# Kernel optimization log

Measured on AMD Instinct MI355X. Metric: run time of the kernel, lower is better.

Reference implementation:

```python
import jax, jax.numpy as jnp
import numpy as np
from jax import lax

DEPTH_MAX = 6.0
NBINS = 100


def _minpool2d(x):
    # torch: -max_pool2d(-x, 5, 1, 2)  (max_pool pads with -inf => minpool pads with +inf)
    return lax.reduce_window(x, jnp.inf, lax.min, (1, 5, 5), (1, 1, 1),
                             [(0, 0), (2, 2), (2, 2)])


def _maxpool3d(x):
    return lax.reduce_window(x, -jnp.inf, lax.max, (1, 5, 5, 5), (1, 1, 1, 1),
                             [(0, 0), (2, 2), (2, 2), (2, 2)])


def _stuff_padding(row, maxvec):
    # fill zeros of `row` with the first nonzero element of `maxvec`
    v = maxvec[jnp.argmax(maxvec != 0)]  # if all-zero, argmax->0, v=0 (no-op fill)
    return jnp.where(row == 0, v, row)


def _find_none(a):
    # Sequential nearest-nonzero fill: for each zero (left->right), set it to
    # max(min nonzero on the left incl. previous fills, min nonzero on the right
    # of the ORIGINAL array). Expressed as a parallel suffix-min + lax.scan.
    aval = jnp.where(a != 0, a, jnp.inf)
    rev = lax.cummin(aval[::-1])[::-1]
    suf = jnp.concatenate([rev[1:], jnp.full((1,), jnp.inf, a.dtype)])  # min of a[i+1:]

    def step(m, xs):
        ai, si = xs
        l = jnp.where(jnp.isinf(m), 0.0, m)
        r = jnp.where(jnp.isinf(si), 0.0, si)
        val = jnp.where(ai == 0, jnp.maximum(l, r), ai)
        m = jnp.where(val != 0, jnp.minimum(m, val), m)
        return m, val

    _, out = lax.scan(step, jnp.array(jnp.inf, a.dtype), (a, suf))
    return out


def _forward(semantic2d, depth, occupancy2d, kept, mapping):
    B, K, H, W = semantic2d.shape
    D = kept.shape[1]
    sem = jnp.argmax(semantic2d, axis=1)               # [B,H,W]
    feats_sm = jax.nn.softmax(semantic2d, axis=1)      # [B,K,H,W]

    depth = lax.stop_gradient(depth)                   # pred['depth'].detach()
    depth = jnp.minimum(depth, DEPTH_MAX)              # clamp to depth_max
    depth_index = (depth / DEPTH_MAX * 100.0).astype(jnp.int32)  # [B,1,H,W]
    bins = jnp.arange(NBINS, dtype=jnp.int32)[None, :, None, None]

    # stuff mask: erosion (min-pool 5x5) of (semantic >= 10)
    stuff = _minpool2d((sem >= 10).astype(depth.dtype)) > 0.5    # [B,H,W] bool
    stuff_depth = depth[:, 0] * stuff                            # [B,H,W]
    stuff_x_max = stuff_depth.max(axis=1)                        # [B,W]
    stuff_y_max = stuff_depth.max(axis=2)                        # [B,H]

    pad_v = jax.vmap(_stuff_padding)
    sd = stuff_depth
    sd = sd.at[:, 0].set(pad_v(stuff_depth[:, 0], stuff_y_max))
    sd = sd.at[:, -1].set(pad_v(stuff_depth[:, -1], stuff_y_max[:, ::-1]))
    sd = sd.at[:, :, 0].set(pad_v(stuff_depth[:, :, 0], stuff_x_max))
    sd = sd.at[:, :, -1].set(pad_v(stuff_depth[:, :, -1], stuff_x_max[:, ::-1]))

    stuff_x = jax.vmap(_find_none)(sd.max(axis=1))   # [B,W]
    stuff_y = jax.vmap(_find_none)(sd.max(axis=2))   # [B,H]

    # per-pixel max depth: min(stuff_x[b, x], stuff_y[b, y])
    depth_max = jnp.minimum(stuff_x[:, None, None, :], stuff_y[:, None, :, None])  # [B,1,H,W]
    depth_max_bins = (depth_max / DEPTH_MAX * 100.0).astype(jnp.int32)

    depth_feat = (bins - depth_index).astype(depth.dtype) / 100.0 * DEPTH_MAX  # [B,100,H,W]
    depth_feat = jnp.stack([jnp.sign(depth_feat), jnp.abs(depth_feat)], axis=1)  # [B,2,100,H,W]

    depth_weight_kept = (bins > depth_index - 3) & (bins < depth_max_bins + 5)  # [B,100,H,W]
    depth_weight = jax.nn.sigmoid(occupancy2d) * depth_weight_kept

    # voxel -> pixel/bin gather: mapping columns are (batch, x, y, depth_m)
    b_idx = mapping[..., 0].astype(jnp.int32)
    x_idx = mapping[..., 1].astype(jnp.int32)
    y_idx = mapping[..., 2].astype(jnp.int32)
    d_idx = (mapping[..., 3] * 100.0 / DEPTH_MAX).astype(jnp.int32)
    feat_kept = kept & depth_weight_kept[b_idx, d_idx, y_idx, x_idx]  # [B,D,D,D]

    features = jnp.concatenate([
        jnp.broadcast_to(feats_sm[:, :, None], (B, K, NBINS, H, W)),
        depth_weight[:, None],
        depth_feat,
    ], axis=1)  # [B, K+3, 100, H, W]

    # padding voxels: dilation of feat_kept within kept, coords snapped to even
    padding_kept = (_maxpool3d(feat_kept.astype(jnp.float32)) > 0.5) & kept
    batch_point = padding_kept.reshape(B, -1).sum(-1)
    padding_kept = padding_kept.at[:, 127, 127, 127].set(
        jnp.where(batch_point == 0, True, padding_kept[:, 127, 127, 127]))
    padding_kept = padding_kept & ~feat_kept
    blocks = padding_kept.reshape(B, D // 2, 2, D // 2, 2, D // 2, 2).any(axis=(2, 4, 6))
    padding_even = jnp.zeros_like(padding_kept).at[:, ::2, ::2, ::2].set(blocks)

    union = feat_kept | padding_even          # occupied sparse coords (dense form)
    mask = _maxpool3d(union.astype(jnp.float32)) > 0.5
    return features, feat_kept, mask


def setup_inputs() -> dict:
    key = jax.random.key(0)
    ks = jax.random.split(key, 7)
    B, K, H, W, D = 2, 12, 120, 160, 128
    semantic2d = jax.random.normal(ks[0], (B, K, H, W), jnp.float32)
    depth = jax.random.uniform(ks[1], (B, 1, H, W), jnp.float32) * 8.0  # some > depth_max
    occupancy2d = jax.random.normal(ks[2], (B, 100, H, W), jnp.float32)
    kept = jax.random.uniform(ks[3], (B, D, D, D)) < 0.05
    b_col = jnp.broadcast_to(jnp.arange(B, dtype=jnp.float32)[:, None, None, None], (B, D, D, D))
    x_col = jax.random.randint(ks[4], (B, D, D, D), 0, W).astype(jnp.float32)
    y_col = jax.random.randint(ks[5], (B, D, D, D), 0, H).astype(jnp.float32)
    d_col = jax.random.uniform(ks[6], (B, D, D, D)) * (DEPTH_MAX - 1e-3)
    mapping = jnp.stack([b_col, x_col, y_col, d_col], axis=-1)  # [B,D,D,D,4]
    return {"semantic2d": semantic2d, "depth": depth, "occupancy2d": occupancy2d,
            "kept": kept, "mapping": mapping}


def reference(semantic2d, depth, occupancy2d, kept, mapping):
    return _forward(semantic2d, depth, occupancy2d, kept, mapping)
```

## Files before the change

### kernel.cpp

```cpp
#include <hip/hip_runtime.h>
#include <cmath>

#define BB 2
#define KK 12
#define HH 120
#define WW 160
#define HW (HH*WW)
#define DD 128
#define NB 100
#define DMAXF 6.0f
#define NLINES (BB*DD*DD)
#define NVOX (BB*DD*DD*DD)

__global__ void k1_pixel(const float* __restrict__ sem2d, const float* __restrict__ depth,
                         float* __restrict__ feats_sm, float* __restrict__ stuffflag,
                         int* __restrict__ di_arr) {
    int t = blockIdx.x * blockDim.x + threadIdx.x;
    if (t >= BB * HW) return;
    int b = t / HW, p = t - b * HW;
    const float* sp = sem2d + (size_t)b * KK * HW + p;
    float v[KK];
    float mx = -INFINITY; int am = 0;
#pragma unroll
    for (int k = 0; k < KK; k++) {
        v[k] = sp[(size_t)k * HW];
        if (v[k] > mx) { mx = v[k]; am = k; }
    }
    float s = 0.f;
#pragma unroll
    for (int k = 0; k < KK; k++) { v[k] = expf(v[k] - mx); s += v[k]; }
    float inv = 1.f / s;
    float* fp = feats_sm + (size_t)b * KK * HW + p;
#pragma unroll
    for (int k = 0; k < KK; k++) fp[(size_t)k * HW] = v[k] * inv;
    stuffflag[t] = (am >= 10) ? 1.f : 0.f;
    float d = fminf(depth[t], DMAXF);
    di_arr[t] = (int)((d / DMAXF) * 100.0f);
}

__global__ void k2_erode(const float* __restrict__ stuffflag, const float* __restrict__ depth,
                         float* __restrict__ stuff_depth) {
    int t = blockIdx.x * blockDim.x + threadIdx.x;
    if (t >= BB * HW) return;
    int b = t / HW, p = t - b * HW;
    int h = p / WW, w = p - h * WW;
    bool all1 = true;
    for (int dh = -2; dh <= 2; dh++) {
        int hh = h + dh; if (hh < 0 || hh >= HH) continue;
        for (int dw = -2; dw <= 2; dw++) {
            int ww = w + dw; if (ww < 0 || ww >= WW) continue;
            all1 = all1 && (stuffflag[b * HW + hh * WW + ww] > 0.5f);
        }
    }
    float d = fminf(depth[t], DMAXF);
    stuff_depth[t] = all1 ? d : 0.f;
}

__global__ void k3_lines(const float* __restrict__ sd, float* __restrict__ stuff_x,
                         float* __restrict__ stuff_y) {
    __shared__ float ymax[HH], xmax[WW], colmax[WW], rowmax[HH];
    __shared__ float sfxc[WW], sfxr[HH];
    __shared__ float vv[4];
    int b = blockIdx.x;
    int t = threadIdx.x;
    const float* base = sd + (size_t)b * HW;

    if (t < HH) { float m = -INFINITY; for (int w = 0; w < WW; w++) m = fmaxf(m, base[t * WW + w]); ymax[t] = m; }
    if (t < WW) { float m = -INFINITY; for (int h = 0; h < HH; h++) m = fmaxf(m, base[h * WW + t]); xmax[t] = m; }
    __syncthreads();

    if (t == 0) {
        float f = 0.f, l = 0.f;
        for (int h = 0; h < HH; h++) { if (ymax[h] != 0.f) { f = ymax[h]; break; } }
        for (int h = HH - 1; h >= 0; h--) { if (ymax[h] != 0.f) { l = ymax[h]; break; } }
        vv[0] = f; vv[1] = l;
    }
    if (t == 1) {
        float f = 0.f, l = 0.f;
        for (int w = 0; w < WW; w++) { if (xmax[w] != 0.f) { f = xmax[w]; break; } }
        for (int w = WW - 1; w >= 0; w--) { if (xmax[w] != 0.f) { l = xmax[w]; break; } }
        vv[2] = f; vv[3] = l;
    }
    __syncthreads();
    float v1 = vv[0], v2 = vv[1], v3 = vv[2], v4 = vv[3];

    auto sdval = [&](int h, int w) -> float {
        float x = base[h * WW + w];
        if (w == 0)      return (x == 0.f) ? v3 : x;
        if (w == WW - 1) return (x == 0.f) ? v4 : x;
        if (h == 0)      return (x == 0.f) ? v1 : x;
        if (h == HH - 1) return (x == 0.f) ? v2 : x;
        return x;
    };
    if (t < WW) { float m = -INFINITY; for (int h = 0; h < HH; h++) m = fmaxf(m, sdval(h, t)); colmax[t] = m; }
    if (t < HH) { float m = -INFINITY; for (int w = 0; w < WW; w++) m = fmaxf(m, sdval(t, w)); rowmax[t] = m; }
    __syncthreads();

    if (t == 0) {
        float m = INFINITY;
        for (int i = WW - 1; i >= 0; i--) { sfxc[i] = m; float a = colmax[i]; if (a != 0.f) m = fminf(m, a); }
        m = INFINITY;
        for (int i = 0; i < WW; i++) {
            float a = colmax[i];
            float l = (m == INFINITY) ? 0.f : m;
            float r = (sfxc[i] == INFINITY) ? 0.f : sfxc[i];
            float val = (a == 0.f) ? fmaxf(l, r) : a;
            if (val != 0.f) m = fminf(m, val);
            stuff_x[b * WW + i] = val;
        }
    }
    if (t == 1) {
        float m = INFINITY;
        for (int i = HH - 1; i >= 0; i--) { sfxr[i] = m; float a = rowmax[i]; if (a != 0.f) m = fminf(m, a); }
        m = INFINITY;
        for (int i = 0; i < HH; i++) {
            float a = rowmax[i];
            float l = (m == INFINITY) ? 0.f : m;
            float r = (sfxr[i] == INFINITY) ? 0.f : sfxr[i];
            float val = (a == 0.f) ? fmaxf(l, r) : a;
            if (val != 0.f) m = fminf(m, val);
            stuff_y[b * HH + i] = val;
        }
    }
}

__global__ void k3b_dmb(const float* __restrict__ stuff_x, const float* __restrict__ stuff_y,
                        int* __restrict__ dmb_arr) {
    int t = blockIdx.x * blockDim.x + threadIdx.x;
    if (t >= BB * HW) return;
    int b = t / HW, p = t - b * HW;
    int h = p / WW, w = p - h * WW;
    float dm = fminf(stuff_x[b * WW + w], stuff_y[b * HH + h]);
    dmb_arr[t] = (int)((dm / DMAXF) * 100.0f);
}

__global__ void k4_features(const float* __restrict__ occ, const float* __restrict__ feats_sm,
                            const int* __restrict__ di_arr, const int* __restrict__ dmb_arr,
                            float* __restrict__ out) {
    int t = blockIdx.x * blockDim.x + threadIdx.x;
    if (t >= BB * NB * HW) return;
    int b = t / (NB * HW);
    int r = t - b * NB * HW;
    int bin = r / HW;
    int p = r - bin * HW;
    int di = di_arr[b * HW + p];
    int db = dmb_arr[b * HW + p];
    float o = occ[t];
    bool dwk = (bin > di - 3) && (bin < db + 5);
    float sg = 1.f / (1.f + expf(-o));
    float dw = dwk ? sg : 0.f;
    float df = ((float)(bin - di)) / 100.0f * DMAXF;
    float sgn = (float)((bin > di) - (bin < di));
    size_t base = ((size_t)b * 15 * NB + bin) * HW + p;
    const float* fp = feats_sm + (size_t)b * KK * HW + p;
#pragma unroll
    for (int c = 0; c < KK; c++) out[base + (size_t)c * NB * HW] = fp[(size_t)c * HW];
    out[base + (size_t)12 * NB * HW] = dw;
    out[base + (size_t)13 * NB * HW] = sgn;
    out[base + (size_t)14 * NB * HW] = fabsf(df);
}

__global__ void k5_gather(const int* __restrict__ kept, const float4* __restrict__ mapping,
                          const int* __restrict__ di_arr, const int* __restrict__ dmb_arr,
                          float* __restrict__ out_fk, unsigned int* __restrict__ fk_pk,
                          unsigned int* __restrict__ kept_pk) {
    int v = blockIdx.x * blockDim.x + threadIdx.x;
    float4 m = mapping[v];
    int bi = (int)m.x, xi = (int)m.y, yi = (int)m.z;
    int dIdx = (int)((m.w * 100.0f) / DMAXF);
    int kp = kept[v];
    int pp = bi * HW + yi * WW + xi;
    int di = di_arr[pp], db = dmb_arr[pp];
    bool dwk = (dIdx > di - 3) && (dIdx < db + 5);
    bool fk = (kp != 0) && dwk;
    out_fk[v] = fk ? 1.f : 0.f;
    unsigned long long mb = __ballot(fk);
    unsigned long long mk = __ballot(kp != 0);
    int lane = threadIdx.x & 63;
    if (lane == 0)  { fk_pk[v >> 5] = (unsigned int)mb;         kept_pk[v >> 5] = (unsigned int)mk; }
    if (lane == 32) { fk_pk[v >> 5] = (unsigned int)(mb >> 32); kept_pk[v >> 5] = (unsigned int)(mk >> 32); }
}

__device__ inline void kdil128(unsigned int w0, unsigned int w1, unsigned int w2, unsigned int w3,
                               unsigned int* r) {
    unsigned int a0 = w0, a1 = w1, a2 = w2, a3 = w3;
    a0 |= w0 << 1; a1 |= (w1 << 1) | (w0 >> 31); a2 |= (w2 << 1) | (w1 >> 31); a3 |= (w3 << 1) | (w2 >> 31);
    a0 |= w0 << 2; a1 |= (w1 << 2) | (w0 >> 30); a2 |= (w2 << 2) | (w1 >> 30); a3 |= (w3 << 2) | (w2 >> 30);
    a0 |= (w0 >> 1) | (w1 << 31); a1 |= (w1 >> 1) | (w2 << 31); a2 |= (w2 >> 1) | (w3 << 31); a3 |= w3 >> 1;
    a0 |= (w0 >> 2) | (w1 << 30); a1 |= (w1 >> 2) | (w2 << 30); a2 |= (w2 >> 2) | (w3 << 30); a3 |= w3 >> 2;
    r[0] = a0; r[1] = a1; r[2] = a2; r[3] = a3;
}

__global__ void k6_dil_jk(const uint4* __restrict__ in, uint4* __restrict__ outb) {
    int l = blockIdx.x * blockDim.x + threadIdx.x;
    if (l >= NLINES) return;
    int b = l / (DD * DD); int rem = l - b * DD * DD; int i = rem / DD; int j = rem - i * DD;
    unsigned int a0 = 0, a1 = 0, a2 = 0, a3 = 0;
    for (int dj = -2; dj <= 2; dj++) {
        int jj = j + dj; if (jj < 0 || jj >= DD) continue;
        uint4 x = in[(b * DD + i) * DD + jj];
        a0 |= x.x; a1 |= x.y; a2 |= x.z; a3 |= x.w;
    }
    unsigned int r[4];
    kdil128(a0, a1, a2, a3, r);
    outb[l] = make_uint4(r[0], r[1], r[2], r[3]);
}

__global__ void k7_dil_i_count(const uint4* __restrict__ tmp1, const uint4* __restrict__ kept_pk,
                               uint4* __restrict__ pad0, int* __restrict__ counters) {
    int l = blockIdx.x * blockDim.x + threadIdx.x;
    if (l >= NLINES) return;
    int b = l / (DD * DD); int rem = l - b * DD * DD; int i = rem / DD; int j = rem - i * DD;
    unsigned int a0 = 0, a1 = 0, a2 = 0, a3 = 0;
    for (int di = -2; di <= 2; di++) {
        int ii = i + di; if (ii < 0 || ii >= DD) continue;
        uint4 x = tmp1[(b * DD + ii) * DD + j];
        a0 |= x.x; a1 |= x.y; a2 |= x.z; a3 |= x.w;
    }
    uint4 kk = kept_pk[l];
    a0 &= kk.x; a1 &= kk.y; a2 &= kk.z; a3 &= kk.w;
    pad0[l] = make_uint4(a0, a1, a2, a3);
    int c = __popc(a0) + __popc(a1) + __popc(a2) + __popc(a3);
    for (int off = 32; off; off >>= 1) c += __shfl_down(c, off);
    if ((threadIdx.x & 63) == 0) atomicAdd(&counters[b], c);
}

__global__ void k8a_finalize(uint4* __restrict__ pad, const uint4* __restrict__ fk_pk,
                             const int* __restrict__ counters) {
    int l = blockIdx.x * blockDim.x + threadIdx.x;
    if (l >= NLINES) return;
    int b = l / (DD * DD); int rem = l - b * DD * DD; int i = rem / DD; int j = rem - i * DD;
    uint4 p = pad[l];
    if (counters[b] == 0 && i == 127 && j == 127) p.w |= 0x80000000u;
    uint4 f = fk_pk[l];
    p.x &= ~f.x; p.y &= ~f.y; p.z &= ~f.z; p.w &= ~f.w;
    pad[l] = p;
}

__global__ void k8b_union(const uint4* __restrict__ pad, const uint4* __restrict__ fk_pk,
                          uint4* __restrict__ uni) {
    int l = blockIdx.x * blockDim.x + threadIdx.x;
    if (l >= NLINES) return;
    int b = l / (DD * DD); int rem = l - b * DD * DD; int i = rem / DD; int j = rem - i * DD;
    uint4 u = fk_pk[l];
    if (((i | j) & 1) == 0) {
        uint4 la = pad[(b * DD + i) * DD + j];
        uint4 lb = pad[(b * DD + i) * DD + j + 1];
        uint4 lc = pad[(b * DD + i + 1) * DD + j];
        uint4 ld = pad[(b * DD + i + 1) * DD + j + 1];
        unsigned int q0 = la.x | lb.x | lc.x | ld.x;
        unsigned int q1 = la.y | lb.y | lc.y | ld.y;
        unsigned int q2 = la.z | lb.z | lc.z | ld.z;
        unsigned int q3 = la.w | lb.w | lc.w | ld.w;
        q0 = (q0 | (q0 >> 1)) & 0x55555555u;
        q1 = (q1 | (q1 >> 1)) & 0x55555555u;
        q2 = (q2 | (q2 >> 1)) & 0x55555555u;
        q3 = (q3 | (q3 >> 1)) & 0x55555555u;
        u.x |= q0; u.y |= q1; u.z |= q2; u.w |= q3;
    }
    uni[l] = u;
}

__global__ void k10_dil_i(const uint4* __restrict__ tmp1, uint4* __restrict__ outb) {
    int l = blockIdx.x * blockDim.x + threadIdx.x;
    if (l >= NLINES) return;
    int b = l / (DD * DD); int rem = l - b * DD * DD; int i = rem / DD; int j = rem - i * DD;
    unsigned int a0 = 0, a1 = 0, a2 = 0, a3 = 0;
    for (int di = -2; di <= 2; di++) {
        int ii = i + di; if (ii < 0 || ii >= DD) continue;
        uint4 x = tmp1[(b * DD + ii) * DD + j];
        a0 |= x.x; a1 |= x.y; a2 |= x.z; a3 |= x.w;
    }
    outb[l] = make_uint4(a0, a1, a2, a3);
}

__global__ void k11_unpack(const unsigned int* __restrict__ mp, float* __restrict__ outm) {
    int v = blockIdx.x * blockDim.x + threadIdx.x;
    if (v >= NVOX) return;
    outm[v] = ((mp[v >> 5] >> (v & 31)) & 1u) ? 1.f : 0.f;
}

extern "C" void kernel_launch(void* const* d_in, const int* in_sizes, int n_in,
                              void* d_out, int out_size, void* d_ws, size_t ws_size,
                              hipStream_t stream) {
    (void)in_sizes; (void)n_in; (void)out_size; (void)ws_size;
    const float* sem2d   = (const float*)d_in[0];
    const float* depth   = (const float*)d_in[1];
    const float* occ     = (const float*)d_in[2];
    const int*   kept    = (const int*)d_in[3];
    const float* mapping = (const float*)d_in[4];
    float* out = (float*)d_out;

    float* feats_sm    = (float*)d_ws;
    float* stuffflag   = feats_sm + BB * KK * HW;
    float* stuff_depth = stuffflag + BB * HW;
    int*   di_arr      = (int*)(stuff_depth + BB * HW);
    int*   dmb_arr     = di_arr + BB * HW;
    float* stuff_x     = (float*)(dmb_arr + BB * HW);
    float* stuff_y     = stuff_x + BB * WW;
    unsigned int* fk_pk   = (unsigned int*)(stuff_y + BB * HH);
    unsigned int* kept_pk = fk_pk + NVOX / 32;
    unsigned int* tmp1    = kept_pk + NVOX / 32;
    unsigned int* pad0    = tmp1 + NVOX / 32;
    unsigned int* uni     = pad0 + NVOX / 32;
    int* counters = (int*)(uni + NVOX / 32);

    hipMemsetAsync(counters, 0, BB * sizeof(int), stream);

    int pixBlocks = (BB * HW + 255) / 256;
    k1_pixel<<<pixBlocks, 256, 0, stream>>>(sem2d, depth, feats_sm, stuffflag, di_arr);
    k2_erode<<<pixBlocks, 256, 0, stream>>>(stuffflag, depth, stuff_depth);
    k3_lines<<<BB, 256, 0, stream>>>(stuff_depth, stuff_x, stuff_y);
    k3b_dmb<<<pixBlocks, 256, 0, stream>>>(stuff_x, stuff_y, dmb_arr);

    k4_features<<<(BB * NB * HW + 255) / 256, 256, 0, stream>>>(occ, feats_sm, di_arr, dmb_arr, out);

    k5_gather<<<NVOX / 256, 256, 0, stream>>>(kept, (const float4*)mapping, di_arr, dmb_arr,
                                              out + (size_t)57600000, fk_pk, kept_pk);

    int lineBlocks = (NLINES + 255) / 256;
    k6_dil_jk<<<lineBlocks, 256, 0, stream>>>((const uint4*)fk_pk, (uint4*)tmp1);
    k7_dil_i_count<<<lineBlocks, 256, 0, stream>>>((const uint4*)tmp1, (const uint4*)kept_pk,
                                                   (uint4*)pad0, counters);
    k8a_finalize<<<lineBlocks, 256, 0, stream>>>((uint4*)pad0, (const uint4*)fk_pk, counters);
    k8b_union<<<lineBlocks, 256, 0, stream>>>((const uint4*)pad0, (const uint4*)fk_pk, (uint4*)uni);
    k6_dil_jk<<<lineBlocks, 256, 0, stream>>>((const uint4*)uni, (uint4*)tmp1);
    k10_dil_i<<<lineBlocks, 256, 0, stream>>>((const uint4*)tmp1, (uint4*)pad0);
    k11_unpack<<<NVOX / 256, 256, 0, stream>>>(pad0, out + (size_t)61794304);
}
```

Measured before the change: 532.3 us.

## Fuse stuff-mask stages, vectorize feature writes, merge dilation and unpack kernels

Erosion, line reductions and the depth-max-bin computation now run in one per-batch kernel. The stuff mask is packed into bitmasks in shared memory, so the intermediate global stuff-depth array and two launches go away. The feature kernel moves to float4 loads and stores with a fast exp. The finalize and union kernels are merged, the last i-dilation is fused into the float unpack, and the counter memset is replaced by a reset inside the first dilation kernel, with the count switched to an atomicOr flag. The cost is that the fused stuff kernel runs on only two blocks and does its serial scans there.

```diff
diff --git a/kernel.cpp b/kernel.cpp
--- a/kernel.cpp
+++ b/kernel.cpp
@@ -11,6 +11,7 @@
 #define DMAXF 6.0f
 #define NLINES (BB*DD*DD)
 #define NVOX (BB*DD*DD*DD)
+#define SDP 161
 
 __global__ void k1_pixel(const float* __restrict__ sem2d, const float* __restrict__ depth,
                          float* __restrict__ feats_sm, float* __restrict__ stuffflag,
@@ -38,35 +39,66 @@
     di_arr[t] = (int)((d / DMAXF) * 100.0f);
 }
 
-__global__ void k2_erode(const float* __restrict__ stuffflag, const float* __restrict__ depth,
-                         float* __restrict__ stuff_depth) {
-    int t = blockIdx.x * blockDim.x + threadIdx.x;
-    if (t >= BB * HW) return;
-    int b = t / HW, p = t - b * HW;
-    int h = p / WW, w = p - h * WW;
-    bool all1 = true;
-    for (int dh = -2; dh <= 2; dh++) {
-        int hh = h + dh; if (hh < 0 || hh >= HH) continue;
-        for (int dw = -2; dw <= 2; dw++) {
-            int ww = w + dw; if (ww < 0 || ww >= WW) continue;
-            all1 = all1 && (stuffflag[b * HW + hh * WW + ww] > 0.5f);
+__global__ __launch_bounds__(256) void k23_stuff(const float* __restrict__ stuffflag,
+                                                 const float* __restrict__ depth,
+                                                 int* __restrict__ dmb_arr) {
+    __shared__ float sd[HH * SDP];
+    __shared__ unsigned int bA[600];
+    __shared__ unsigned int bB[600];
+    __shared__ float ymax[HH], xmax[WW], colmax[WW], rowmax[HH];
+    __shared__ float sufc[WW], sufr[HH];
+    __shared__ float sxv[WW], syv[HH];
+    __shared__ float vv[4];
+    int b = blockIdx.x, t = threadIdx.x;
+    const float* sf = stuffflag + b * HW;
+    const float* dp = depth + b * HW;
+
+    for (int it = 0; it < HW / 256; ++it) {
+        int p = it * 256 + t;
+        bool fl = sf[p] > 0.5f;
+        unsigned long long m = __ballot(fl);
+        int lane = t & 63;
+        if (lane == 0)  bA[p >> 5] = (unsigned int)m;
+        if (lane == 32) bA[p >> 5] = (unsigned int)(m >> 32);
+    }
+    __syncthreads();
+
+    for (int q = t; q < 600; q += 256) {
+        int w = q % 5;
+        unsigned int cur = bA[q];
+        unsigned int left  = (w > 0) ? bA[q - 1] : 0xFFFFFFFFu;
+        unsigned int right = (w < 4) ? bA[q + 1] : 0xFFFFFFFFu;
+        unsigned int sL1 = (cur >> 1) | (right << 31);
+        unsigned int sL2 = (cur >> 2) | (right << 30);
+        unsigned int sR1 = (cur << 1) | (left >> 31);
+        unsigned int sR2 = (cur << 2) | (left >> 30);
+        bB[q] = cur & sL1 & sL2 & sR1 & sR2;
+    }
+    __syncthreads();
+
+    for (int q = t; q < 600; q += 256) {
+        int h = q / 5, w = q - h * 5;
+        unsigned int v = 0xFFFFFFFFu;
+#pragma unroll
+        for (int dh = -2; dh <= 2; ++dh) {
+            int hh = h + dh;
+            if (hh >= 0 && hh < HH) v &= bB[hh * 5 + w];
         }
-    }
-    float d = fminf(depth[t], DMAXF);
-    stuff_depth[t] = all1 ? d : 0.f;
-}
-
-__global__ void k3_lines(const float* __restrict__ sd, float* __restrict__ stuff_x,
-                         float* __restrict__ stuff_y) {
-    __shared__ float ymax[HH], xmax[WW], colmax[WW], rowmax[HH];
-    __shared__ float sfxc[WW], sfxr[HH];
-    __shared__ float vv[4];
-    int b = blockIdx.x;
-    int t = threadIdx.x;
-    const float* base = sd + (size_t)b * HW;
-
-    if (t < HH) { float m = -INFINITY; for (int w = 0; w < WW; w++) m = fmaxf(m, base[t * WW + w]); ymax[t] = m; }
-    if (t < WW) { float m = -INFINITY; for (int h = 0; h < HH; h++) m = fmaxf(m, base[h * WW + t]); xmax[t] = m; }
+        bA[q] = v;
+    }
+    __syncthreads();
+
+    for (int it = 0; it < HW / 256; ++it) {
+        int p = it * 256 + t;
+        int h = p / WW, w = p - h * WW;
+        unsigned int bit = (bA[p >> 5] >> (p & 31)) & 1u;
+        float d = fminf(dp[p], DMAXF);
+        sd[h * SDP + w] = bit ? d : 0.f;
+    }
+    __syncthreads();
+
+    if (t < HH) { float m = -INFINITY; for (int w = 0; w < WW; w++) m = fmaxf(m, sd[t * SDP + w]); ymax[t] = m; }
+    if (t < WW) { float m = -INFINITY; for (int h = 0; h < HH; h++) m = fmaxf(m, sd[h * SDP + t]); xmax[t] = m; }
     __syncthreads();
 
     if (t == 0) {
@@ -85,7 +117,7 @@
     float v1 = vv[0], v2 = vv[1], v3 = vv[2], v4 = vv[3];
 
     auto sdval = [&](int h, int w) -> float {
-        float x = base[h * WW + w];
+        float x = sd[h * SDP + w];
         if (w == 0)      return (x == 0.f) ? v3 : x;
         if (w == WW - 1) return (x == 0.f) ? v4 : x;
         if (h == 0)      return (x == 0.f) ? v1 : x;
@@ -98,66 +130,74 @@
 
     if (t == 0) {
         float m = INFINITY;
-        for (int i = WW - 1; i >= 0; i--) { sfxc[i] = m; float a = colmax[i]; if (a != 0.f) m = fminf(m, a); }
+        for (int i = WW - 1; i >= 0; i--) { sufc[i] = m; float a = colmax[i]; if (a != 0.f) m = fminf(m, a); }
         m = INFINITY;
         for (int i = 0; i < WW; i++) {
             float a = colmax[i];
             float l = (m == INFINITY) ? 0.f : m;
-            float r = (sfxc[i] == INFINITY) ? 0.f : sfxc[i];
+            float r = (sufc[i] == INFINITY) ? 0.f : sufc[i];
             float val = (a == 0.f) ? fmaxf(l, r) : a;
             if (val != 0.f) m = fminf(m, val);
-            stuff_x[b * WW + i] = val;
+            sxv[i] = val;
         }
     }
     if (t == 1) {
         float m = INFINITY;
-        for (int i = HH - 1; i >= 0; i--) { sfxr[i] = m; float a = rowmax[i]; if (a != 0.f) m = fminf(m, a); }
+        for (int i = HH - 1; i >= 0; i--) { sufr[i] = m; float a = rowmax[i]; if (a != 0.f) m = fminf(m, a); }
         m = INFINITY;
         for (int i = 0; i < HH; i++) {
             float a = rowmax[i];
             float l = (m == INFINITY) ? 0.f : m;
-            float r = (sfxr[i] == INFINITY) ? 0.f : sfxr[i];
+            float r = (sufr[i] == INFINITY) ? 0.f : sufr[i];
             float val = (a == 0.f) ? fmaxf(l, r) : a;
             if (val != 0.f) m = fminf(m, val);
-            stuff_y[b * HH + i] = val;
+            syv[i] = val;
         }
     }
-}
-
-__global__ void k3b_dmb(const float* __restrict__ stuff_x, const float* __restrict__ stuff_y,
-                        int* __restrict__ dmb_arr) {
+    __syncthreads();
+
+    for (int it = 0; it < HW / 256; ++it) {
+        int p = it * 256 + t;
+        int h = p / WW, w = p - h * WW;
+        float dm = fminf(sxv[w], syv[h]);
+        dmb_arr[b * HW + p] = (int)((dm / DMAXF) * 100.0f);
+    }
+}
+
+__device__ inline void comp1(float o, int di, int db, int bin, float& dw, float& sg, float& ad) {
+    bool dwk = (bin > di - 3) && (bin < db + 5);
+    float s = 1.f / (1.f + __expf(-o));
+    dw = dwk ? s : 0.f;
+    float df = ((float)(bin - di)) / 100.0f * DMAXF;
+    sg = (float)((bin > di) - (bin < di));
+    ad = fabsf(df);
+}
+
+__global__ void k4_features(const float4* __restrict__ occ4, const float4* __restrict__ fs4,
+                            const int4* __restrict__ di4, const int4* __restrict__ dmb4,
+                            float4* __restrict__ out4) {
+    const int HW4 = HW / 4;
     int t = blockIdx.x * blockDim.x + threadIdx.x;
-    if (t >= BB * HW) return;
-    int b = t / HW, p = t - b * HW;
-    int h = p / WW, w = p - h * WW;
-    float dm = fminf(stuff_x[b * WW + w], stuff_y[b * HH + h]);
-    dmb_arr[t] = (int)((dm / DMAXF) * 100.0f);
-}
-
-__global__ void k4_features(const float* __restrict__ occ, const float* __restrict__ feats_sm,
-                            const int* __restrict__ di_arr, const int* __restrict__ dmb_arr,
-                            float* __restrict__ out) {
-    int t = blockIdx.x * blockDim.x + threadIdx.x;
-    if (t >= BB * NB * HW) return;
-    int b = t / (NB * HW);
-    int r = t - b * NB * HW;
-    int bin = r / HW;
-    int p = r - bin * HW;
-    int di = di_arr[b * HW + p];
-    int db = dmb_arr[b * HW + p];
-    float o = occ[t];
-    bool dwk = (bin > di - 3) && (bin < db + 5);
-    float sg = 1.f / (1.f + expf(-o));
-    float dw = dwk ? sg : 0.f;
-    float df = ((float)(bin - di)) / 100.0f * DMAXF;
-    float sgn = (float)((bin > di) - (bin < di));
-    size_t base = ((size_t)b * 15 * NB + bin) * HW + p;
-    const float* fp = feats_sm + (size_t)b * KK * HW + p;
-#pragma unroll
-    for (int c = 0; c < KK; c++) out[base + (size_t)c * NB * HW] = fp[(size_t)c * HW];
-    out[base + (size_t)12 * NB * HW] = dw;
-    out[base + (size_t)13 * NB * HW] = sgn;
-    out[base + (size_t)14 * NB * HW] = fabsf(df);
+    if (t >= BB * NB * HW4) return;
+    int b = t / (NB * HW4);
+    int r = t - b * (NB * HW4);
+    int bin = r / HW4;
+    int p4 = r - bin * HW4;
+    int4 di = di4[b * HW4 + p4];
+    int4 db = dmb4[b * HW4 + p4];
+    float4 o = occ4[t];
+    float4 dw, sgn, adf;
+    comp1(o.x, di.x, db.x, bin, dw.x, sgn.x, adf.x);
+    comp1(o.y, di.y, db.y, bin, dw.y, sgn.y, adf.y);
+    comp1(o.z, di.z, db.z, bin, dw.z, sgn.z, adf.z);
+    comp1(o.w, di.w, db.w, bin, dw.w, sgn.w, adf.w);
+    size_t base = (size_t)(b * 15 * NB + bin) * HW4 + p4;
+    const float4* fp = fs4 + (size_t)b * KK * HW4 + p4;
+#pragma unroll
+    for (int c = 0; c < KK; c++) out4[base + (size_t)c * NB * HW4] = fp[(size_t)c * HW4];
+    out4[base + (size_t)12 * NB * HW4] = dw;
+    out4[base + (size_t)13 * NB * HW4] = sgn;
+    out4[base + (size_t)14 * NB * HW4] = adf;
 }
 
 __global__ void k5_gather(const int* __restrict__ kept, const float4* __restrict__ mapping,
@@ -191,11 +231,13 @@
     r[0] = a0; r[1] = a1; r[2] = a2; r[3] = a3;
 }
 
-__global__ void k6_dil_jk(const uint4* __restrict__ in, uint4* __restrict__ outb) {
+__global__ void k6_dil_jk(const uint4* __restrict__ in, uint4* __restrict__ outb,
+                          int* __restrict__ counters) {
     int l = blockIdx.x * blockDim.x + threadIdx.x;
-    if (l >= NLINES) return;
+    if (l == 0) { counters[0] = 0; counters[1] = 0; }
     int b = l / (DD * DD); int rem = l - b * DD * DD; int i = rem / DD; int j = rem - i * DD;
     unsigned int a0 = 0, a1 = 0, a2 = 0, a3 = 0;
+#pragma unroll
     for (int dj = -2; dj <= 2; dj++) {
         int jj = j + dj; if (jj < 0 || jj >= DD) continue;
         uint4 x = in[(b * DD + i) * DD + jj];
@@ -209,9 +251,9 @@
 __global__ void k7_dil_i_count(const uint4* __restrict__ tmp1, const uint4* __restrict__ kept_pk,
                                uint4* __restrict__ pad0, int* __restrict__ counters) {
     int l = blockIdx.x * blockDim.x + threadIdx.x;
-    if (l >= NLINES) return;
     int b = l / (DD * DD); int rem = l - b * DD * DD; int i = rem / DD; int j = rem - i * DD;
     unsigned int a0 = 0, a1 = 0, a2 = 0, a3 = 0;
+#pragma unroll
     for (int di = -2; di <= 2; di++) {
         int ii = i + di; if (ii < 0 || ii >= DD) continue;
         uint4 x = tmp1[(b * DD + ii) * DD + j];
@@ -220,38 +262,29 @@
     uint4 kk = kept_pk[l];
     a0 &= kk.x; a1 &= kk.y; a2 &= kk.z; a3 &= kk.w;
     pad0[l] = make_uint4(a0, a1, a2, a3);
-    int c = __popc(a0) + __popc(a1) + __popc(a2) + __popc(a3);
-    for (int off = 32; off; off >>= 1) c += __shfl_down(c, off);
-    if ((threadIdx.x & 63) == 0) atomicAdd(&counters[b], c);
-}
-
-__global__ void k8a_finalize(uint4* __restrict__ pad, const uint4* __restrict__ fk_pk,
-                             const int* __restrict__ counters) {
+    unsigned long long bal = __ballot((a0 | a1 | a2 | a3) != 0u);
+    if ((threadIdx.x & 63) == 0 && bal) atomicOr(&counters[b], 1);
+}
+
+__global__ void k8ab_union(const uint4* __restrict__ pad0, const uint4* __restrict__ fk_pk,
+                           const int* __restrict__ counters, uint4* __restrict__ uni) {
     int l = blockIdx.x * blockDim.x + threadIdx.x;
-    if (l >= NLINES) return;
-    int b = l / (DD * DD); int rem = l - b * DD * DD; int i = rem / DD; int j = rem - i * DD;
-    uint4 p = pad[l];
-    if (counters[b] == 0 && i == 127 && j == 127) p.w |= 0x80000000u;
-    uint4 f = fk_pk[l];
-    p.x &= ~f.x; p.y &= ~f.y; p.z &= ~f.z; p.w &= ~f.w;
-    pad[l] = p;
-}
-
-__global__ void k8b_union(const uint4* __restrict__ pad, const uint4* __restrict__ fk_pk,
-                          uint4* __restrict__ uni) {
-    int l = blockIdx.x * blockDim.x + threadIdx.x;
-    if (l >= NLINES) return;
-    int b = l / (DD * DD); int rem = l - b * DD * DD; int i = rem / DD; int j = rem - i * DD;
+    int b = l >> 14; int rem = l & 16383; int i = rem >> 7; int j = rem & 127;
     uint4 u = fk_pk[l];
     if (((i | j) & 1) == 0) {
-        uint4 la = pad[(b * DD + i) * DD + j];
-        uint4 lb = pad[(b * DD + i) * DD + j + 1];
-        uint4 lc = pad[(b * DD + i + 1) * DD + j];
-        uint4 ld = pad[(b * DD + i + 1) * DD + j + 1];
-        unsigned int q0 = la.x | lb.x | lc.x | ld.x;
-        unsigned int q1 = la.y | lb.y | lc.y | ld.y;
-        unsigned int q2 = la.z | lb.z | lc.z | ld.z;
-        unsigned int q3 = la.w | lb.w | lc.w | ld.w;
+        bool c0 = (counters[b] == 0);
+        unsigned int q0 = 0, q1 = 0, q2 = 0, q3 = 0;
+#pragma unroll
+        for (int di2 = 0; di2 < 2; di2++)
+#pragma unroll
+            for (int dj2 = 0; dj2 < 2; dj2++) {
+                int ii = i + di2, jj = j + dj2;
+                int ll = (b * DD + ii) * DD + jj;
+                uint4 p = pad0[ll]; uint4 f = fk_pk[ll];
+                unsigned int pw = p.w;
+                if (c0 && ii == 127 && jj == 127) pw |= 0x80000000u;
+                q0 |= p.x & ~f.x; q1 |= p.y & ~f.y; q2 |= p.z & ~f.z; q3 |= pw & ~f.w;
+            }
         q0 = (q0 | (q0 >> 1)) & 0x55555555u;
         q1 = (q1 | (q1 >> 1)) & 0x55555555u;
         q2 = (q2 | (q2 >> 1)) & 0x55555555u;
@@ -261,23 +294,25 @@
     uni[l] = u;
 }
 
-__global__ void k10_dil_i(const uint4* __restrict__ tmp1, uint4* __restrict__ outb) {
-    int l = blockIdx.x * blockDim.x + threadIdx.x;
-    if (l >= NLINES) return;
-    int b = l / (DD * DD); int rem = l - b * DD * DD; int i = rem / DD; int j = rem - i * DD;
-    unsigned int a0 = 0, a1 = 0, a2 = 0, a3 = 0;
+__global__ void k11f_dil_unpack(const unsigned int* __restrict__ tmp1w, float4* __restrict__ outm) {
+    int t = blockIdx.x * blockDim.x + threadIdx.x;
+    int vb = t << 2;
+    int line = vb >> 7;
+    int wi = (vb >> 5) & 3;
+    int bo = vb & 31;
+    int b = line >> 14; int rem = line & 16383; int i = rem >> 7; int j = rem & 127;
+    unsigned int w = 0;
+#pragma unroll
     for (int di = -2; di <= 2; di++) {
-        int ii = i + di; if (ii < 0 || ii >= DD) continue;
-        uint4 x = tmp1[(b * DD + ii) * DD + j];
-        a0 |= x.x; a1 |= x.y; a2 |= x.z; a3 |= x.w;
-    }
-    outb[l] = make_uint4(a0, a1, a2, a3);
-}
-
-__global__ void k11_unpack(const unsigned int* __restrict__ mp, float* __restrict__ outm) {
-    int v = blockIdx.x * blockDim.x + threadIdx.x;
-    if (v >= NVOX) return;
-    outm[v] = ((mp[v >> 5] >> (v & 31)) & 1u) ? 1.f : 0.f;
+        int ii = i + di;
+        if (ii >= 0 && ii < DD) w |= tmp1w[((b * DD + ii) * DD + j) * 4 + wi];
+    }
+    float4 r;
+    r.x = (float)((w >> bo) & 1u);
+    r.y = (float)((w >> (bo + 1)) & 1u);
+    r.z = (float)((w >> (bo + 2)) & 1u);
+    r.w = (float)((w >> (bo + 3)) & 1u);
+    outm[t] = r;
 }
 
 extern "C" void kernel_launch(void* const* d_in, const int* in_sizes, int n_in,
@@ -293,38 +328,31 @@
 
     float* feats_sm    = (float*)d_ws;
     float* stuffflag   = feats_sm + BB * KK * HW;
-    float* stuff_depth = stuffflag + BB * HW;
-    int*   di_arr      = (int*)(stuff_depth + BB * HW);
+    int*   di_arr      = (int*)(stuffflag + BB * HW);
     int*   dmb_arr     = di_arr + BB * HW;
-    float* stuff_x     = (float*)(dmb_arr + BB * HW);
-    float* stuff_y     = stuff_x + BB * WW;
-    unsigned int* fk_pk   = (unsigned int*)(stuff_y + BB * HH);
+    unsigned int* fk_pk   = (unsigned int*)(dmb_arr + BB * HW);
     unsigned int* kept_pk = fk_pk + NVOX / 32;
     unsigned int* tmp1    = kept_pk + NVOX / 32;
     unsigned int* pad0    = tmp1 + NVOX / 32;
     unsigned int* uni     = pad0 + NVOX / 32;
     int* counters = (int*)(uni + NVOX / 32);
 
-    hipMemsetAsync(counters, 0, BB * sizeof(int), stream);
-
-    int pixBlocks = (BB * HW + 255) / 256;
-    k1_pixel<<<pixBlocks, 256, 0, stream>>>(sem2d, depth, feats_sm, stuffflag, di_arr);
-    k2_erode<<<pixBlocks, 256, 0, stream>>>(stuffflag, depth, stuff_depth);
-    k3_lines<<<BB, 256, 0, stream>>>(stuff_depth, stuff_x, stuff_y);
-    k3b_dmb<<<pixBlocks, 256, 0, stream>>>(stuff_x, stuff_y, dmb_arr);
-
-    k4_features<<<(BB * NB * HW + 255) / 256, 256, 0, stream>>>(occ, feats_sm, di_arr, dmb_arr, out);
+    k1_pixel<<<BB * HW / 256, 256, 0, stream>>>(sem2d, depth, feats_sm, stuffflag, di_arr);
+    k23_stuff<<<BB, 256, 0, stream>>>(stuffflag, depth, dmb_arr);
+
+    k4_features<<<BB * NB * (HW / 4) / 256, 256, 0, stream>>>(
+        (const float4*)occ, (const float4*)feats_sm, (const int4*)di_arr, (const int4*)dmb_arr,
+        (float4*)out);
 
     k5_gather<<<NVOX / 256, 256, 0, stream>>>(kept, (const float4*)mapping, di_arr, dmb_arr,
                                               out + (size_t)57600000, fk_pk, kept_pk);
 
-    int lineBlocks = (NLINES + 255) / 256;
-    k6_dil_jk<<<lineBlocks, 256, 0, stream>>>((const uint4*)fk_pk, (uint4*)tmp1);
+    int lineBlocks = NLINES / 256;
+    k6_dil_jk<<<lineBlocks, 256, 0, stream>>>((const uint4*)fk_pk, (uint4*)tmp1, counters);
     k7_dil_i_count<<<lineBlocks, 256, 0, stream>>>((const uint4*)tmp1, (const uint4*)kept_pk,
                                                    (uint4*)pad0, counters);
-    k8a_finalize<<<lineBlocks, 256, 0, stream>>>((uint4*)pad0, (const uint4*)fk_pk, counters);
-    k8b_union<<<lineBlocks, 256, 0, stream>>>((const uint4*)pad0, (const uint4*)fk_pk, (uint4*)uni);
-    k6_dil_jk<<<lineBlocks, 256, 0, stream>>>((const uint4*)uni, (uint4*)tmp1);
-    k10_dil_i<<<lineBlocks, 256, 0, stream>>>((const uint4*)tmp1, (uint4*)pad0);
-    k11_unpack<<<NVOX / 256, 256, 0, stream>>>(pad0, out + (size_t)61794304);
-}
+    k8ab_union<<<lineBlocks, 256, 0, stream>>>((const uint4*)pad0, (const uint4*)fk_pk, counters,
+                                               (uint4*)uni);
+    k6_dil_jk<<<lineBlocks, 256, 0, stream>>>((const uint4*)uni, (uint4*)tmp1, counters);
+    k11f_dil_unpack<<<NVOX / 4 / 256, 256, 0, stream>>>(tmp1, (float4*)(out + (size_t)61794304));
+}
```

Result: faster. 521.3 us (-2.1%).
